# Kernel optimization log

Measured on AMD Instinct MI355X. Metric: run time of the kernel, lower is better.

## Reference

```python
import jax, jax.numpy as jnp
import numpy as np

EPS = 1e-3  # keras LayerNormalization default epsilon


def _ln(x, g, b):
    m = jnp.mean(x, axis=-1, keepdims=True)
    v = jnp.mean(jnp.square(x - m), axis=-1, keepdims=True)
    return (x - m) * jax.lax.rsqrt(v + EPS) * g + b


def setup_inputs() -> dict:
    key = jax.random.key(0)
    B, T, C, H = 64, 256, 1024, 16
    D = C // H
    ks = jax.random.split(key, 16)
    s = 0.02
    return {
        "x": jax.random.normal(ks[0], (B, T, C), jnp.float32),
        # per-head q/k/v projections (no bias), stacked over heads [H, C, D]
        "wq": jax.random.normal(ks[1], (H, C, D), jnp.float32) * s,
        "wk": jax.random.normal(ks[2], (H, C, D), jnp.float32) * s,
        "wv": jax.random.normal(ks[3], (H, C, D), jnp.float32) * s,
        "w_proj": jax.random.normal(ks[4], (C, C), jnp.float32) * s,
        "b_proj": jnp.zeros((C,), jnp.float32),
        # FFN: C -> 4C (relu) -> C
        "w1": jax.random.normal(ks[5], (C, 4 * C), jnp.float32) * s,
        "b1": jnp.zeros((4 * C,), jnp.float32),
        "w2": jax.random.normal(ks[6], (4 * C, C), jnp.float32) * s,
        "b2": jnp.zeros((C,), jnp.float32),
        # LayerNorm params: ln1 (pre-attn), ln2 (pre-ffn), ln3 (inside FeedForward)
        "g1": jnp.ones((C,), jnp.float32), "be1": jnp.zeros((C,), jnp.float32),
        "g2": jnp.ones((C,), jnp.float32), "be2": jnp.zeros((C,), jnp.float32),
        "g3": jnp.ones((C,), jnp.float32), "be3": jnp.zeros((C,), jnp.float32),
    }


def reference(x, wq, wk, wv, w_proj, b_proj, w1, b1, w2, b2,
              g1, be1, g2, be2, g3, be3):
    B, T, C = x.shape
    # --- multi-head causal self-attention on LN1(x) ---
    h = _ln(x, g1, be1)
    q = jnp.einsum('btc,hcd->bhtd', h, wq)
    k = jnp.einsum('btc,hcd->bhtd', h, wk)
    v = jnp.einsum('btc,hcd->bhtd', h, wv)
    # NOTE: original scales by C**-0.5 with C = n_embd (full dim), not head_size
    scores = jnp.einsum('bhtd,bhsd->bhts', q, k) * (C ** -0.5)
    causal = jnp.tril(jnp.ones((T, T), dtype=bool))
    scores = jnp.where(causal, scores, -jnp.inf)
    attn = jax.nn.softmax(scores, axis=-1)  # dropout is identity at inference
    out = jnp.einsum('bhts,bhsd->bhtd', attn, v)
    out = out.transpose(0, 2, 1, 3).reshape(B, T, C)  # concat heads
    out = out @ w_proj + b_proj
    x = x + out
    # --- FeedForward block (contains its own residual + LayerNorm) ---
    y = _ln(x, g2, be2)
    z = jax.nn.relu(y @ w1 + b1) @ w2 + b2
    return x + _ln(y + z, g3, be3)
```

## Files before the change

kernel.cpp:

```cpp
#include <hip/hip_runtime.h>

typedef __bf16 bf16_t;
typedef __bf16 bf16x8 __attribute__((ext_vector_type(8)));
typedef float f32x4 __attribute__((ext_vector_type(4)));

#define LN_EPS 1e-3f

__device__ __forceinline__ void gload_lds16(const void* g, void* l) {
    __builtin_amdgcn_global_load_lds(
        (__attribute__((address_space(1))) void*)(g),
        (__attribute__((address_space(3))) void*)(l), 16, 0, 0);
}

__global__ __launch_bounds__(256)
void transpose_f32_bf16(const float* __restrict__ in, bf16_t* __restrict__ outp,
                        int ldi, int ldo)
{
    __shared__ float tile[64][65];
    const int k0 = blockIdx.x * 64, n0 = blockIdx.y * 64;
    const int tid = threadIdx.x;
    const int r = tid >> 2;
    const int q = tid & 3;
    const float* src = in + (long)(k0 + r) * ldi + n0 + q * 16;
#pragma unroll
    for (int j = 0; j < 4; ++j) {
        float4 v = *(const float4*)(src + j * 4);
        tile[r][q * 16 + j * 4 + 0] = v.x;
        tile[r][q * 16 + j * 4 + 1] = v.y;
        tile[r][q * 16 + j * 4 + 2] = v.z;
        tile[r][q * 16 + j * 4 + 3] = v.w;
    }
    __syncthreads();
    union { bf16_t e[16]; uint4 u[2]; } pk;
#pragma unroll
    for (int j = 0; j < 16; ++j) pk.e[j] = (bf16_t)tile[q * 16 + j][r];
    bf16_t* dst = outp + (long)(n0 + r) * ldo + k0 + q * 16;
    *(uint4*)(dst)     = pk.u[0];
    *(uint4*)(dst + 8) = pk.u[1];
}

__global__ __launch_bounds__(256)
void pack_qkv_t(const float* __restrict__ wq, const float* __restrict__ wk,
                const float* __restrict__ wv, bf16_t* __restrict__ outp)
{
    __shared__ float tile[64][65];
    const int m   = blockIdx.y;
    const int sel = m >> 4, h = m & 15;
    const float* in = ((sel == 0) ? wq : (sel == 1) ? wk : wv) + (long)h * 65536;
    bf16_t* out = outp + ((long)sel * 1024 + h * 64) * 1024;
    const int k0 = blockIdx.x * 64;
    const int tid = threadIdx.x;
    const int r = tid >> 2;
    const int q = tid & 3;
    const float* src = in + (long)(k0 + r) * 64 + q * 16;
#pragma unroll
    for (int j = 0; j < 4; ++j) {
        float4 v = *(const float4*)(src + j * 4);
        tile[r][q * 16 + j * 4 + 0] = v.x;
        tile[r][q * 16 + j * 4 + 1] = v.y;
        tile[r][q * 16 + j * 4 + 2] = v.z;
        tile[r][q * 16 + j * 4 + 3] = v.w;
    }
    __syncthreads();
    union { bf16_t e[16]; uint4 u[2]; } pk;
#pragma unroll
    for (int j = 0; j < 16; ++j) pk.e[j] = (bf16_t)tile[q * 16 + j][r];
    bf16_t* dst = out + (long)r * 1024 + k0 + q * 16;
    *(uint4*)(dst)     = pk.u[0];
    *(uint4*)(dst + 8) = pk.u[1];
}

__global__ __launch_bounds__(256)
void v_transpose(const bf16_t* __restrict__ qkv, bf16_t* __restrict__ vt)
{
    int g  = blockIdx.x * 256 + threadIdx.x;
    int bh = g >> 11;
    int r  = g & 2047;
    int d  = r & 63;
    int sg = r >> 6;
    int b  = bh >> 4, h = bh & 15;
    const bf16_t* src = qkv + ((long)b * 256 + sg * 8) * 3072 + 2048 + h * 64 + d;
    union { bf16_t e[8]; uint4 u; } pk;
#pragma unroll
    for (int e = 0; e < 8; ++e) pk.e[e] = src[(long)e * 3072];
    *(uint4*)(vt + ((long)bh * 64 + d) * 256 + sg * 8) = pk.u;
}

__global__ __launch_bounds__(256)
void ln_fwd(const float* __restrict__ in, const float* __restrict__ g,
            const float* __restrict__ be, bf16_t* __restrict__ outp)
{
    const long row = blockIdx.x;
    const int t = threadIdx.x;
    float4 v = ((const float4*)(in + row * 1024))[t];
    float s  = v.x + v.y + v.z + v.w;
    float sq = v.x * v.x + v.y * v.y + v.z * v.z + v.w * v.w;
#pragma unroll
    for (int off = 1; off < 64; off <<= 1) {
        s  += __shfl_xor(s, off);
        sq += __shfl_xor(sq, off);
    }
    __shared__ float red[8];
    if ((t & 63) == 0) { red[(t >> 6) * 2] = s; red[(t >> 6) * 2 + 1] = sq; }
    __syncthreads();
    s  = red[0] + red[2] + red[4] + red[6];
    sq = red[1] + red[3] + red[5] + red[7];
    float mean = s * 0.0009765625f;
    float var  = sq * 0.0009765625f - mean * mean;
    float rstd = rsqrtf(var + LN_EPS);
    float4 gv = ((const float4*)g)[t];
    float4 bv = ((const float4*)be)[t];
    union { bf16_t h[4]; uint2 u; } pk;
    pk.h[0] = (bf16_t)((v.x - mean) * rstd * gv.x + bv.x);
    pk.h[1] = (bf16_t)((v.y - mean) * rstd * gv.y + bv.y);
    pk.h[2] = (bf16_t)((v.z - mean) * rstd * gv.z + bv.z);
    pk.h[3] = (bf16_t)((v.w - mean) * rstd * gv.w + bv.w);
    *(uint2*)(outp + row * 1024 + t * 4) = pk.u;
}

__global__ __launch_bounds__(256)
void ln3_kernel(const bf16_t* __restrict__ in, const float* __restrict__ g,
                const float* __restrict__ be, float* outp, const float* res)
{
    const long row = blockIdx.x;
    const int t = threadIdx.x;
    union { uint2 u; bf16_t h[4]; } pk;
    pk.u = *(const uint2*)(in + row * 1024 + t * 4);
    float v0 = (float)pk.h[0], v1 = (float)pk.h[1], v2 = (float)pk.h[2], v3 = (float)pk.h[3];
    float s  = v0 + v1 + v2 + v3;
    float sq = v0 * v0 + v1 * v1 + v2 * v2 + v3 * v3;
#pragma unroll
    for (int off = 1; off < 64; off <<= 1) {
        s  += __shfl_xor(s, off);
        sq += __shfl_xor(sq, off);
    }
    __shared__ float red[8];
    if ((t & 63) == 0) { red[(t >> 6) * 2] = s; red[(t >> 6) * 2 + 1] = sq; }
    __syncthreads();
    s  = red[0] + red[2] + red[4] + red[6];
    sq = red[1] + red[3] + red[5] + red[7];
    float mean = s * 0.0009765625f;
    float var  = sq * 0.0009765625f - mean * mean;
    float rstd = rsqrtf(var + LN_EPS);
    float4 gv = ((const float4*)g)[t];
    float4 bv = ((const float4*)be)[t];
    float4 rv = ((const float4*)(res + row * 1024))[t];
    float4 ov;
    ov.x = rv.x + (v0 - mean) * rstd * gv.x + bv.x;
    ov.y = rv.y + (v1 - mean) * rstd * gv.y + bv.y;
    ov.z = rv.z + (v2 - mean) * rstd * gv.z + bv.z;
    ov.w = rv.w + (v3 - mean) * rstd * gv.w + bv.w;
    ((float4*)outp)[row * 256 + t] = ov;
}

template<int MODE>
__global__ __launch_bounds__(512, 2)
void gemm_bt(const bf16_t* __restrict__ Ap, const bf16_t* __restrict__ Bp,
             void* outp, const float* __restrict__ bias,
             const void* addp, int M, int N, int K)
{
    __shared__ __attribute__((aligned(16))) bf16_t As0[256 * 64];
    __shared__ __attribute__((aligned(16))) bf16_t As1[256 * 64];
    __shared__ __attribute__((aligned(16))) bf16_t Bs0[256 * 64];
    __shared__ __attribute__((aligned(16))) bf16_t Bs1[256 * 64];

    const int tid  = threadIdx.x;
    const int w    = tid >> 6, lane = tid & 63;
    const int l16  = lane & 15, lg = lane >> 4;
    const int wm   = w >> 2, wn = w & 3;
    const int srow = lane >> 3;
    const int sslot = lane & 7;

    const int gx  = gridDim.x;
    const int gy  = gridDim.y;
    const int nwg = gx * gy;
    const int bid = blockIdx.y * gx + blockIdx.x;
    const int cpx = nwg >> 3;
    const int sid = (bid & 7) * cpx + (bid >> 3);
    const long m0 = (long)(sid / gy) * 256;
    const long n0 = (long)(sid % gy) * 256;
    const int nkt = K >> 6;

    f32x4 acc[8][4] = {};
    bf16x8 a[4][2], b0[2][2], b1[2][2];

    auto STAGEH = [&](const bf16_t* src, long row0, int kt, bf16_t* dst, int h) {
#pragma unroll
        for (int i = 0; i < 2; ++i) {
            int r  = h * 128 + w * 16 + i * 8 + srow;
            int ss = sslot ^ (r & 7);
            gload_lds16(src + (row0 + r) * (long)K + (long)kt * 64 + ss * 8,
                        dst + (h * 128 + w * 16 + i * 8) * 64);
        }
    };

#define LDA_M(buf, mh) do {                                               \
    _Pragma("unroll") for (int j = 0; j < 4; ++j)                         \
    _Pragma("unroll") for (int kk = 0; kk < 2; ++kk) {                    \
        int r  = wm * 128 + (mh) * 64 + j * 16 + l16;                     \
        int ss = (kk * 4 + lg) ^ (r & 7);                                 \
        a[j][kk] = *(const bf16x8*)&buf[r * 64 + ss * 8];                 \
    } } while (0)

#define LDB_M(dst, buf, nh) do {                                          \
    _Pragma("unroll") for (int n = 0; n < 2; ++n)                         \
    _Pragma("unroll") for (int kk = 0; kk < 2; ++kk) {                    \
        int r  = wn * 64 + ((nh) * 2 + n) * 16 + l16;                     \
        int ss = (kk * 4 + lg) ^ (r & 7);                                 \
        dst[n][kk] = *(const bf16x8*)&buf[r * 64 + ss * 8];               \
    } } while (0)

#define MMA_M(bv, mh, nh) do {                                            \
    __builtin_amdgcn_s_setprio(1);                                        \
    _Pragma("unroll") for (int j = 0; j < 4; ++j)                         \
    _Pragma("unroll") for (int n = 0; n < 2; ++n)                         \
    _Pragma("unroll") for (int kk = 0; kk < 2; ++kk)                      \
        acc[(mh) * 4 + j][(nh) * 2 + n] =                                 \
            __builtin_amdgcn_mfma_f32_16x16x32_bf16(                      \
                a[j][kk], bv[n][kk], acc[(mh) * 4 + j][(nh) * 2 + n],     \
                0, 0, 0);                                                 \
    __builtin_amdgcn_s_setprio(0);                                        \
} while (0)

#define PRE_MFMA() do { __builtin_amdgcn_s_barrier();                     \
    asm volatile("s_waitcnt lgkmcnt(0)" ::: "memory");                    \
    __builtin_amdgcn_sched_barrier(0); } while (0)

    STAGEH(Ap, m0, 0, As0, 0); STAGEH(Ap, m0, 0, As0, 1);
    STAGEH(Bp, n0, 0, Bs0, 0); STAGEH(Bp, n0, 0, Bs0, 1);
    STAGEH(Ap, m0, 1, As1, 0);
    asm volatile("s_waitcnt vmcnt(2)" ::: "memory");
    __builtin_amdgcn_s_barrier();
    __builtin_amdgcn_sched_barrier(0);

    const int niter = nkt >> 1;
    for (int it = 0; it < niter; ++it) {
        const int c1 = 2 * it + 1, c2 = 2 * it + 2, c3 = 2 * it + 3;
        const bool pf = (c2 < nkt);

        LDA_M(As0, 0); LDB_M(b0, Bs0, 0);
        STAGEH(Ap, m0, c1, As1, 1);
        STAGEH(Bp, n0, c1, Bs1, 0);
        PRE_MFMA(); MMA_M(b0, 0, 0); __builtin_amdgcn_s_barrier();
        LDB_M(b1, Bs0, 1);
        STAGEH(Bp, n0, c1, Bs1, 1);
        PRE_MFMA(); MMA_M(b1, 0, 1); __builtin_amdgcn_s_barrier();
        LDA_M(As0, 1);
        if (pf) STAGEH(Bp, n0, c2, Bs0, 0);
        PRE_MFMA(); MMA_M(b1, 1, 1); __builtin_amdgcn_s_barrier();
        if (pf) {
            STAGEH(Bp, n0, c2, Bs0, 1);
            asm volatile("s_waitcnt vmcnt(4)" ::: "memory");
        } else {
            asm volatile("s_waitcnt vmcnt(0)" ::: "memory");
        }
        __builtin_amdgcn_s_barrier();
        __builtin_amdgcn_sched_barrier(0);
        MMA_M(b0, 1, 0); __builtin_amdgcn_s_barrier();
        LDA_M(As1, 0); LDB_M(b0, Bs1, 0);
        if (pf) STAGEH(Ap, m0, c2, As0, 0);
        PRE_MFMA(); MMA_M(b0, 0, 0); __builtin_amdgcn_s_barrier();
        LDB_M(b1, Bs1, 1);
        if (pf) STAGEH(Ap, m0, c2, As0, 1);
        PRE_MFMA(); MMA_M(b1, 0, 1); __builtin_amdgcn_s_barrier();
        LDA_M(As1, 1);
        PRE_MFMA(); MMA_M(b1, 1, 1); __builtin_amdgcn_s_barrier();
        if (pf) {
            STAGEH(Ap, m0, c3, As1, 0);
            asm volatile("s_waitcnt vmcnt(2)" ::: "memory");
        }
        __builtin_amdgcn_s_barrier();
        __builtin_amdgcn_sched_barrier(0);
        MMA_M(b0, 1, 0); __builtin_amdgcn_s_barrier();
    }

#pragma unroll
    for (int fm = 0; fm < 8; ++fm) {
#pragma unroll
        for (int fn = 0; fn < 4; ++fn) {
            const long gcol = n0 + wn * 64 + fn * 16 + l16;
            float bv = 0.f;
            if (MODE != 0) bv = bias[gcol];
#pragma unroll
            for (int e = 0; e < 4; ++e) {
                const long grow = m0 + wm * 128 + fm * 16 + lg * 4 + e;
                float v = acc[fm][fn][e];
                if (MODE == 0) {
                    ((bf16_t*)outp)[grow * N + gcol] = (bf16_t)v;
                } else if (MODE == 1) {
                    v += bv + ((const float*)addp)[grow * N + gcol];
                    ((float*)outp)[grow * N + gcol] = v;
                } else if (MODE == 2) {
                    v += bv; v = v > 0.f ? v : 0.f;
                    ((bf16_t*)outp)[grow * N + gcol] = (bf16_t)v;
                } else {
                    v += bv + (float)((const bf16_t*)addp)[grow * N + gcol];
                    ((bf16_t*)outp)[grow * N + gcol] = (bf16_t)v;
                }
            }
        }
    }
#undef LDA_M
#undef LDB_M
#undef MMA_M
#undef PRE_MFMA
}

__global__ __launch_bounds__(256)
void attn_kernel(const bf16_t* __restrict__ qkv, const bf16_t* __restrict__ vt,
                 bf16_t* __restrict__ outp)
{
    __shared__ __attribute__((aligned(16))) bf16_t Kt[64 * 64];
    __shared__ __attribute__((aligned(16))) bf16_t Vt[64 * 64];
    __shared__ __attribute__((aligned(16))) bf16_t Ps[4][16 * 72];

    const int tid = threadIdx.x, w = tid >> 6, lane = tid & 63;
    const int l16 = lane & 15, lg = lane >> 4;
    const int b = blockIdx.x >> 4, hh = blockIdx.x & 15;
    const bf16_t* pq = qkv + (long)(b * 256) * 3072 + hh * 64;
    const bf16_t* pv = vt + (long)blockIdx.x * 64 * 256;
    const int sr8 = lane >> 3;
    const int sl  = lane & 7;

    bf16x8 qf[4][2];
#pragma unroll
    for (int fm = 0; fm < 4; ++fm)
#pragma unroll
        for (int kk = 0; kk < 2; ++kk)
            qf[fm][kk] = *(const bf16x8*)(pq + (long)(w * 64 + fm * 16 + l16) * 3072
                                          + kk * 32 + lg * 8);

    f32x4 o[4][4] = {};
    float mrun[4][4], lrun[4][4];
#pragma unroll
    for (int i = 0; i < 4; ++i)
#pragma unroll
        for (int j = 0; j < 4; ++j) { mrun[i][j] = -__builtin_inff(); lrun[i][j] = 0.f; }

    for (int st = 0; st < 4; ++st) {
        __syncthreads();
#pragma unroll
        for (int i = 0; i < 2; ++i) {
            int r  = w * 16 + i * 8 + sr8;
            int ss = sl ^ (r & 7);
            gload_lds16(pq + (long)(st * 64 + r) * 3072 + 1024 + ss * 8,
                        &Kt[(w * 16 + i * 8) * 64]);
            gload_lds16(pv + (long)r * 256 + st * 64 + ss * 8,
                        &Vt[(w * 16 + i * 8) * 64]);
        }
        asm volatile("s_waitcnt vmcnt(0)" ::: "memory");
        __syncthreads();
        if (st > w) continue;

        f32x4 s[4][4] = {};
#pragma unroll
        for (int ks = 0; ks < 2; ++ks) {
            bf16x8 kb[4];
#pragma unroll
            for (int fs = 0; fs < 4; ++fs)
                kb[fs] = *(const bf16x8*)&Kt[(fs * 16 + l16) * 64
                                             + ((ks * 4 + lg) ^ (l16 & 7)) * 8];
#pragma unroll
            for (int fm = 0; fm < 4; ++fm)
#pragma unroll
                for (int fs = 0; fs < 4; ++fs)
                    s[fm][fs] = __builtin_amdgcn_mfma_f32_16x16x32_bf16(
                        qf[fm][ks], kb[fs], s[fm][fs], 0, 0, 0);
        }

#pragma unroll
        for (int fm = 0; fm < 4; ++fm) {
#pragma unroll
            for (int fs = 0; fs < 4; ++fs)
#pragma unroll
                for (int e = 0; e < 4; ++e) {
                    float v = s[fm][fs][e] * 0.03125f;
                    if (st == w && (fs * 16 + l16) > (fm * 16 + lg * 4 + e))
                        v = -__builtin_inff();
                    s[fm][fs][e] = v;
                }
#pragma unroll
            for (int e = 0; e < 4; ++e) {
                float pm = fmaxf(fmaxf(s[fm][0][e], s[fm][1][e]),
                                 fmaxf(s[fm][2][e], s[fm][3][e]));
#pragma unroll
                for (int off = 1; off < 16; off <<= 1) pm = fmaxf(pm, __shfl_xor(pm, off));
                float mnew  = fmaxf(mrun[fm][e], pm);
                float alpha = __expf(mrun[fm][e] - mnew);
                float rs = 0.f;
#pragma unroll
                for (int fs = 0; fs < 4; ++fs) {
                    float p = __expf(s[fm][fs][e] - mnew);
                    s[fm][fs][e] = p;
                    rs += p;
                }
#pragma unroll
                for (int off = 1; off < 16; off <<= 1) rs += __shfl_xor(rs, off);
                lrun[fm][e] = lrun[fm][e] * alpha + rs;
                mrun[fm][e] = mnew;
#pragma unroll
                for (int fd = 0; fd < 4; ++fd) o[fm][fd][e] *= alpha;
            }
#pragma unroll
            for (int fs = 0; fs < 4; ++fs)
#pragma unroll
                for (int e = 0; e < 4; ++e)
                    Ps[w][(lg * 4 + e) * 72 + fs * 16 + l16] = (bf16_t)s[fm][fs][e];
            bf16x8 ap0 = *(const bf16x8*)&Ps[w][l16 * 72 + lg * 8];
            bf16x8 ap1 = *(const bf16x8*)&Ps[w][l16 * 72 + 32 + lg * 8];
#pragma unroll
            for (int fd = 0; fd < 4; ++fd) {
                bf16x8 vb0 = *(const bf16x8*)&Vt[(fd * 16 + l16) * 64
                                                 + ((lg) ^ (l16 & 7)) * 8];
                bf16x8 vb1 = *(const bf16x8*)&Vt[(fd * 16 + l16) * 64
                                                 + ((4 + lg) ^ (l16 & 7)) * 8];
                o[fm][fd] = __builtin_amdgcn_mfma_f32_16x16x32_bf16(ap0, vb0, o[fm][fd], 0, 0, 0);
                o[fm][fd] = __builtin_amdgcn_mfma_f32_16x16x32_bf16(ap1, vb1, o[fm][fd], 0, 0, 0);
            }
        }
    }

#pragma unroll
    for (int fm = 0; fm < 4; ++fm)
#pragma unroll
        for (int e = 0; e < 4; ++e) {
            float inv = 1.f / lrun[fm][e];
            long row = (long)b * 256 + w * 64 + fm * 16 + lg * 4 + e;
#pragma unroll
            for (int fd = 0; fd < 4; ++fd)
                outp[row * 1024 + hh * 64 + fd * 16 + l16] =
                    (bf16_t)(o[fm][fd][e] * inv);
        }
}

extern "C" void kernel_launch(void* const* d_in, const int* in_sizes, int n_in,
                              void* d_out, int out_size, void* d_ws, size_t ws_size,
                              hipStream_t stream)
{
    (void)in_sizes; (void)n_in; (void)out_size; (void)ws_size;
    const float* x      = (const float*)d_in[0];
    const float* wq     = (const float*)d_in[1];
    const float* wk     = (const float*)d_in[2];
    const float* wv     = (const float*)d_in[3];
    const float* w_proj = (const float*)d_in[4];
    const float* b_proj = (const float*)d_in[5];
    const float* w1     = (const float*)d_in[6];
    const float* b1     = (const float*)d_in[7];
    const float* w2     = (const float*)d_in[8];
    const float* b2     = (const float*)d_in[9];
    const float* g1  = (const float*)d_in[10]; const float* be1 = (const float*)d_in[11];
    const float* g2  = (const float*)d_in[12]; const float* be2 = (const float*)d_in[13];
    const float* g3  = (const float*)d_in[14]; const float* be3 = (const float*)d_in[15];

    char* ws = (char*)d_ws;
    bf16_t* wqkv  = (bf16_t*)(ws + 0);
    bf16_t* wproj = (bf16_t*)(ws + 6291456);
    bf16_t* w1t   = (bf16_t*)(ws + 8388608);
    bf16_t* w2t   = (bf16_t*)(ws + 16777216);
    bf16_t* h     = (bf16_t*)(ws + 25165824);
    bf16_t* qkv   = (bf16_t*)(ws + 58720256);
    bf16_t* attn  = h;
    bf16_t* u     = h;
    bf16_t* y     = (bf16_t*)(ws + 159383552);
    bf16_t* vt    = y;
    float*  x2    = (float*)d_out;
    bf16_t* tbuf  = y;

    const int M = 16384;

    transpose_f32_bf16<<<dim3(16, 16), 256, 0, stream>>>(w_proj, wproj, 1024, 1024);
    transpose_f32_bf16<<<dim3(16, 64), 256, 0, stream>>>(w1, w1t, 4096, 1024);
    transpose_f32_bf16<<<dim3(64, 16), 256, 0, stream>>>(w2, w2t, 1024, 4096);
    pack_qkv_t<<<dim3(16, 48), 256, 0, stream>>>(wq, wk, wv, wqkv);

    ln_fwd<<<M, 256, 0, stream>>>(x, g1, be1, h);
    gemm_bt<0><<<dim3(64, 12), 512, 0, stream>>>(h, wqkv, qkv, nullptr, nullptr, M, 3072, 1024);
    v_transpose<<<8192, 256, 0, stream>>>(qkv, vt);
    attn_kernel<<<1024, 256, 0, stream>>>(qkv, vt, attn);
    gemm_bt<1><<<dim3(64, 4), 512, 0, stream>>>(attn, wproj, x2, b_proj, x, M, 1024, 1024);
    ln_fwd<<<M, 256, 0, stream>>>(x2, g2, be2, y);
    gemm_bt<2><<<dim3(64, 16), 512, 0, stream>>>(y, w1t, u, b1, nullptr, M, 4096, 1024);
    gemm_bt<3><<<dim3(64, 4), 512, 0, stream>>>(u, w2t, tbuf, b2, y, M, 1024, 4096);
    ln3_kernel<<<M, 256, 0, stream>>>(tbuf, g3, be3, (float*)d_out, x2);
}
```

Baseline: 681.3 us.

## Triple-buffer A tiles in LDS with prefetch distance two in GEMM

Adds a third LDS buffer for the A operand and restructures the unrolled ping-pong main loop into a single-step loop that rotates buffer pointers. It prefetches A two K-tiles ahead and B one tile ahead. The aim is to hide global load latency better. The extra 32KB of LDS reduces how many workgroups fit per CU, and the changed wait counts make the load ordering more fragile.

```diff
diff --git a/kernel.cpp b/kernel.cpp
--- a/kernel.cpp
+++ b/kernel.cpp
@@ -161,6 +161,7 @@
 {
     __shared__ __attribute__((aligned(16))) bf16_t As0[256 * 64];
     __shared__ __attribute__((aligned(16))) bf16_t As1[256 * 64];
+    __shared__ __attribute__((aligned(16))) bf16_t As2[256 * 64];
     __shared__ __attribute__((aligned(16))) bf16_t Bs0[256 * 64];
     __shared__ __attribute__((aligned(16))) bf16_t Bs1[256 * 64];
 
@@ -228,50 +229,35 @@
 
     STAGEH(Ap, m0, 0, As0, 0); STAGEH(Ap, m0, 0, As0, 1);
     STAGEH(Bp, n0, 0, Bs0, 0); STAGEH(Bp, n0, 0, Bs0, 1);
-    STAGEH(Ap, m0, 1, As1, 0);
-    asm volatile("s_waitcnt vmcnt(2)" ::: "memory");
+    STAGEH(Ap, m0, 1, As1, 0); STAGEH(Ap, m0, 1, As1, 1);
+    asm volatile("s_waitcnt vmcnt(0)" ::: "memory");
     __builtin_amdgcn_s_barrier();
     __builtin_amdgcn_sched_barrier(0);
 
-    const int niter = nkt >> 1;
-    for (int it = 0; it < niter; ++it) {
-        const int c1 = 2 * it + 1, c2 = 2 * it + 2, c3 = 2 * it + 3;
-        const bool pf = (c2 < nkt);
-
-        LDA_M(As0, 0); LDB_M(b0, Bs0, 0);
-        STAGEH(Ap, m0, c1, As1, 1);
-        STAGEH(Bp, n0, c1, Bs1, 0);
+    bf16_t *Ar = As0, *An1 = As1, *An2 = As2;
+    bf16_t *Br = Bs0, *Bw = Bs1;
+
+    for (int c = 0; c < nkt; ++c) {
+        const bool pfa = (c + 2 < nkt);
+        const bool pfb = (c + 1 < nkt);
+
+        LDA_M(Ar, 0); LDB_M(b0, Br, 0);
+        if (pfb) { STAGEH(Bp, n0, c + 1, Bw, 0); STAGEH(Bp, n0, c + 1, Bw, 1); }
+        if (pfa) STAGEH(Ap, m0, c + 2, An2, 0);
         PRE_MFMA(); MMA_M(b0, 0, 0); __builtin_amdgcn_s_barrier();
-        LDB_M(b1, Bs0, 1);
-        STAGEH(Bp, n0, c1, Bs1, 1);
+        LDB_M(b1, Br, 1);
         PRE_MFMA(); MMA_M(b1, 0, 1); __builtin_amdgcn_s_barrier();
-        LDA_M(As0, 1);
-        if (pf) STAGEH(Bp, n0, c2, Bs0, 0);
+        LDA_M(Ar, 1);
+        if (pfa) STAGEH(Ap, m0, c + 2, An2, 1);
         PRE_MFMA(); MMA_M(b1, 1, 1); __builtin_amdgcn_s_barrier();
-        if (pf) {
-            STAGEH(Bp, n0, c2, Bs0, 1);
-            asm volatile("s_waitcnt vmcnt(4)" ::: "memory");
-        } else {
-            asm volatile("s_waitcnt vmcnt(0)" ::: "memory");
-        }
+        if (pfa) { asm volatile("s_waitcnt vmcnt(4)" ::: "memory"); }
+        else     { asm volatile("s_waitcnt vmcnt(0)" ::: "memory"); }
         __builtin_amdgcn_s_barrier();
         __builtin_amdgcn_sched_barrier(0);
         MMA_M(b0, 1, 0); __builtin_amdgcn_s_barrier();
-        LDA_M(As1, 0); LDB_M(b0, Bs1, 0);
-        if (pf) STAGEH(Ap, m0, c2, As0, 0);
-        PRE_MFMA(); MMA_M(b0, 0, 0); __builtin_amdgcn_s_barrier();
-        LDB_M(b1, Bs1, 1);
-        if (pf) STAGEH(Ap, m0, c2, As0, 1);
-        PRE_MFMA(); MMA_M(b1, 0, 1); __builtin_amdgcn_s_barrier();
-        LDA_M(As1, 1);
-        PRE_MFMA(); MMA_M(b1, 1, 1); __builtin_amdgcn_s_barrier();
-        if (pf) {
-            STAGEH(Ap, m0, c3, As1, 0);
-            asm volatile("s_waitcnt vmcnt(2)" ::: "memory");
-        }
-        __builtin_amdgcn_s_barrier();
-        __builtin_amdgcn_sched_barrier(0);
-        MMA_M(b0, 1, 0); __builtin_amdgcn_s_barrier();
+
+        bf16_t* t = Ar; Ar = An1; An1 = An2; An2 = t;
+        t = Br; Br = Bw; Bw = t;
     }
 
 #pragma unroll
```

Result: faster. 655.4 us (-3.8%).
